# Performance work log

Hardware: AMD Instinct MI355X
Metric: run time of the kernel (lower is better)

## Reference

```python
import jax, jax.numpy as jnp
import numpy as np

SIGMA = 0.1
B = 1.0
SPATIAL_WEIGHT = 0.5
EPS = 1e-5


def setup_inputs() -> dict:
    key = jax.random.key(0)
    k1, k2 = jax.random.split(key)
    N, C, H, W = 2, 256, 64, 64
    I_features = jax.random.normal(k1, (N, C, H, W), dtype=jnp.float32)
    T_features = jax.random.normal(k2, (N, C, H, W), dtype=jnp.float32)
    return {"I_features": I_features, "T_features": T_features}


def _calc_cx(raw):
    # raw: [N, P_T, H, W]; min + exp-softmax over the target-patch axis (axis=1)
    mn = jnp.min(raw, axis=1, keepdims=True)
    rel = raw / (mn + EPS)
    w = jnp.exp((B - rel) / SIGMA)
    return w / jnp.sum(w, axis=1, keepdims=True)


def reference(I_features, T_features):
    N, C, H, W = I_features.shape
    P = H * W

    # ---- spatial branch: L2 distances on a normalized meshgrid (C=2) ----
    rows = jnp.arange(H, dtype=jnp.float32) / (H + 1)
    cols = jnp.arange(W, dtype=jnp.float32) / (W + 1)
    grid = jnp.stack(jnp.meshgrid(rows, cols, indexing="ij"))  # [2, H, W]
    g = grid.reshape(2, P)                                      # [2, P]
    sq = jnp.sum(g * g, axis=0)                                 # [P]
    d = sq[:, None] + sq[None, :] - 2.0 * (g.T @ g)             # [P_I, P_T]
    d = jnp.clip(d, 0.0)
    raw_sp = d.T.reshape(1, P, H, W)  # [1, P_T, H, W]; identical per sample
    cx_sp = _calc_cx(raw_sp)

    # ---- feature branch: cosine similarity via centered, L2-normed feats ----
    meanT = jnp.mean(T_features, axis=(0, 2, 3), keepdims=True)
    Ic = I_features - meanT
    Tc = T_features - meanT
    In = Ic / jnp.linalg.norm(Ic, axis=1, keepdims=True)
    Tn = Tc / jnp.linalg.norm(Tc, axis=1, keepdims=True)
    Iv = In.reshape(N, C, P)
    Tv = Tn.reshape(N, C, P)
    dot = jnp.einsum("ncq,ncp->nqp", Tv, Iv)  # [N, P_T, P_I]
    raw_feat = ((1.0 - dot) / 2.0).reshape(N, P, H, W)
    cx_feat = _calc_cx(raw_feat)

    # ---- combine, max over I positions, mean over T patches, -log, mean ----
    cx = (1.0 - SPATIAL_WEIGHT) * cx_feat + SPATIAL_WEIGHT * cx_sp  # [N,P,H,W]
    m = jnp.max(cx, axis=(2, 3))  # [N, P]
    m = jnp.mean(m, axis=1)       # [N]
    return jnp.mean(-jnp.log(m))
```

## Files before the change

### kernel.cpp

```cpp
#include <hip/hip_runtime.h>
#include <math.h>

#define PP 4096
#define CC 256
#define NN 2
#define QS 256
#define NSTEP (PP / QS)

typedef __attribute__((ext_vector_type(4))) float f32x4;

__device__ __forceinline__ void gld_lds16(const char* g, char* l) {
    __builtin_amdgcn_global_load_lds(
        (const __attribute__((address_space(1))) unsigned int*)g,
        (__attribute__((address_space(3))) unsigned int*)l, 16, 0, 0);
}


__global__ __launch_bounds__(256) void mean_kernel(const float* __restrict__ T,
                                                   float* __restrict__ meanT,
                                                   float* __restrict__ loss_acc) {
    int c = blockIdx.x, tid = threadIdx.x;
    float s = 0.f;
    for (int n = 0; n < NN; n++) {
        const float4* Tc = (const float4*)&T[(size_t)(n * CC + c) * PP];
        for (int g = 0; g < 4; g++) {
            float4 v = Tc[tid + g * 256];
            s += (v.x + v.y) + (v.z + v.w);
        }
    }
    __shared__ float red[256];
    red[tid] = s; __syncthreads();
    for (int st = 128; st > 0; st >>= 1) {
        if (tid < st) red[tid] += red[tid + st];
        __syncthreads();
    }
    if (tid == 0) meanT[c] = red[0] * (1.0f / (NN * PP));
    if (blockIdx.x == 0 && tid < NN) loss_acc[tid] = 0.f;
}

__global__ __launch_bounds__(256) void normalize_kernel(const float* __restrict__ I,
                                                        const float* __restrict__ T,
                                                        const float* __restrict__ meanT,
                                                        char* __restrict__ InT,
                                                        char* __restrict__ TnT) {
    int pc = blockIdx.x * 32;
    int n = blockIdx.y;
    int which = blockIdx.z;
    const float* X = which ? T : I;
    char* Y = which ? TnT : InT;

    __shared__ float tile[CC][36];
    __shared__ float red[32][32];
    __shared__ float invn[32];

    int tid = threadIdx.x;
    int pl4 = tid & 7, c0 = tid >> 3;
    float sq0 = 0.f, sq1 = 0.f, sq2 = 0.f, sq3 = 0.f;
    for (int c = c0; c < CC; c += 32) {
        float m = meanT[c];
        float4 v = *(const float4*)&X[(size_t)(n * CC + c) * PP + pc + pl4 * 4];
        v.x -= m; v.y -= m; v.z -= m; v.w -= m;
        *(float4*)&tile[c][pl4 * 4] = v;
        sq0 += v.x * v.x; sq1 += v.y * v.y; sq2 += v.z * v.z; sq3 += v.w * v.w;
    }
    red[c0][pl4 * 4 + 0] = sq0;
    red[c0][pl4 * 4 + 1] = sq1;
    red[c0][pl4 * 4 + 2] = sq2;
    red[c0][pl4 * 4 + 3] = sq3;
    __syncthreads();
    if (tid < 32) {
        float s = 0.f;
        for (int k = 0; k < 32; k++) s += red[k][tid];
        invn[tid] = 1.0f / sqrtf(s);
    }
    __syncthreads();
    for (int pass = 0; pass < 8; pass++) {
        int r = pass * 4 + (tid >> 6);
        int c4 = (tid & 63) * 4;
        float in = invn[r];
        float v0 = tile[c4 + 0][r] * in;
        float v1 = tile[c4 + 1][r] * in;
        float v2 = tile[c4 + 2][r] * in;
        float v3 = tile[c4 + 3][r] * in;
        int w = __builtin_amdgcn_cvt_pk_fp8_f32(v0, v1, 0, false);
        w = __builtin_amdgcn_cvt_pk_fp8_f32(v2, v3, w, true);
        *(unsigned*)&Y[(size_t)(n * PP + pc + r) * CC + c4] = (unsigned)w;
    }
}

__global__ __launch_bounds__(512) void cx_strip(const char* __restrict__ TnT,
                                                const char* __restrict__ InT,
                                                float* __restrict__ loss_acc) {
    const int strip = blockIdx.x;
    const int n = blockIdx.y;
    const int p0 = strip * 32;
    const char* __restrict__ Ab = TnT + (size_t)n * PP * CC;
    const char* __restrict__ Bb = InT + (size_t)n * PP * CC + (size_t)p0 * CC;

    __shared__ __align__(16) char As[2][QS * 256];
    __shared__ __align__(16) char Bs[32 * 256];
    __shared__ float redw[8][32];
    __shared__ float inv2s[32];
    __shared__ float dwl[32];

    const int tid = threadIdx.x;
    const int l = tid & 63, wv = tid >> 6;
    const int lm = l & 15, quad = l >> 4;

    const int srl = tid >> 4;
    const int sch = ((tid & 15) ^ (srl & 15)) * 16;
    const char* Asrc = Ab + srl * 256 + sch;
    char* Alds = (char*)As + tid * 16;

    gld_lds16(Bb + srl * 256 + sch, (char*)Bs + tid * 16);

    long bf[2][8];
    float cm[2] = {3.4e38f, 3.4e38f};
    float inv2[2] = {0.f, 0.f};
    float ss[2] = {0.f, 0.f};
    const int qd = p0 >> 8;
    const int wd = (p0 >> 5) & 7;

#pragma unroll 1
    for (int pass = 0; pass < 2; pass++) {
#pragma unroll
        for (int g = 0; g < 8; g++)
            gld_lds16(Asrc + g * 8192, Alds + g * 8192);
        __syncthreads();

        if (pass == 0) {
#pragma unroll
            for (int ct = 0; ct < 2; ct++)
#pragma unroll
                for (int ks = 0; ks < 8; ks++) {
                    int g8 = ks * 4 + quad;
                    int row = ct * 16 + lm;
                    bf[ct][ks] = *(const long*)&Bs[row * 256 +
                                  (((g8 >> 1) ^ (row & 15)) * 16) + (g8 & 1) * 8];
                }
        }

#pragma unroll 1
        for (int qs = 0; qs < NSTEP; qs++) {
            if (qs < NSTEP - 1) {
                const char* s = Asrc + (size_t)(qs + 1) * 65536;
                char* d = Alds + ((qs + 1) & 1) * 65536;
#pragma unroll
                for (int g = 0; g < 8; g++)
                    gld_lds16(s + g * 8192, d + g * 8192);
            }

            const char* Ac = (const char*)As + (qs & 1) * 65536;
            f32x4 acc[2][2] = {};
#pragma unroll
            for (int ks = 0; ks < 8; ks++) {
                const int off = (((ks * 2 + (quad >> 1)) ^ lm) * 16) + (quad & 1) * 8;
                long a[2];
#pragma unroll
                for (int i = 0; i < 2; i++)
                    a[i] = *(const long*)&Ac[(wv * 32 + i * 16 + lm) * 256 + off];
#pragma unroll
                for (int i = 0; i < 2; i++)
#pragma unroll
                    for (int ct = 0; ct < 2; ct++)
                        acc[i][ct] = __builtin_amdgcn_mfma_f32_16x16x32_fp8_fp8(
                            a[i], bf[ct][ks], acc[i][ct], 0, 0, 0);
            }
            if (pass == 0) {
#pragma unroll
                for (int ct = 0; ct < 2; ct++)
#pragma unroll
                    for (int i = 0; i < 2; i++)
#pragma unroll
                        for (int e = 0; e < 4; e++)
                            cm[ct] = fminf(cm[ct], (1.0f - acc[i][ct][e]) * 0.5f);
            } else {
                const bool dstep = (qs == qd) && (wv == wd);
#pragma unroll
                for (int ct = 0; ct < 2; ct++) {
                    float s2 = 0.f;
#pragma unroll
                    for (int i = 0; i < 2; i++)
#pragma unroll
                        for (int e = 0; e < 4; e++) {
                            float raw = (1.0f - acc[i][ct][e]) * 0.5f;
                            float w = exp2f(fmaf(raw, -inv2[ct], 14.4269504f));
                            s2 += w;
                            if (dstep && (i * 16 + quad * 4 + e == ct * 16 + lm))
                                dwl[ct * 16 + lm] = w;
                        }
                    ss[ct] += s2;
                }
            }
            __syncthreads();
        }

        if (pass == 0) {
#pragma unroll
            for (int ct = 0; ct < 2; ct++) {
                cm[ct] = fminf(cm[ct], __shfl_xor(cm[ct], 16));
                cm[ct] = fminf(cm[ct], __shfl_xor(cm[ct], 32));
                if (quad == 0) redw[wv][ct * 16 + lm] = cm[ct];
            }
            __syncthreads();
            if (tid < 32) {
                float m = redw[0][tid];
#pragma unroll
                for (int w2 = 1; w2 < 8; w2++) m = fminf(m, redw[w2][tid]);
                inv2s[tid] = 14.4269504f / (m + 1e-5f);
            }
            __syncthreads();
            inv2[0] = inv2s[lm];
            inv2[1] = inv2s[16 + lm];
        }
    }

#pragma unroll
    for (int ct = 0; ct < 2; ct++) {
        ss[ct] += __shfl_xor(ss[ct], 16);
        ss[ct] += __shfl_xor(ss[ct], 32);
        if (quad == 0) redw[wv][ct * 16 + lm] = ss[ct];
    }
    __syncthreads();
    if (tid < 32) {
        float s = 0.f;
#pragma unroll
        for (int w2 = 0; w2 < 8; w2++) s += redw[w2][tid];
        float part = dwl[tid] / s;
        part += __shfl_xor(part, 1);
        part += __shfl_xor(part, 2);
        part += __shfl_xor(part, 4);
        part += __shfl_xor(part, 8);
        part += __shfl_xor(part, 16);
        if (tid == 0) atomicAdd(&loss_acc[n], part);
    }
}

__global__ void finalize_kernel(const float* __restrict__ loss_acc,
                                float* __restrict__ out) {
    float m0 = 0.5f + 0.5f * (loss_acc[0] / (float)PP);
    float m1 = 0.5f + 0.5f * (loss_acc[1] / (float)PP);
    out[0] = 0.5f * (-logf(m0) - logf(m1));
}

extern "C" void kernel_launch(void* const* d_in, const int* in_sizes, int n_in,
                              void* d_out, int out_size, void* d_ws, size_t ws_size,
                              hipStream_t stream) {
    const float* I = (const float*)d_in[0];
    const float* T = (const float*)d_in[1];
    float* out = (float*)d_out;

    char* ws = (char*)d_ws;
    const size_t SZ_F8 = (size_t)NN * PP * CC;
    char* InT = ws;
    char* TnT = ws + SZ_F8;
    float* meanT = (float*)(ws + 2 * SZ_F8);
    float* loss_acc = (float*)(ws + 2 * SZ_F8 + 32768);

    mean_kernel<<<CC, 256, 0, stream>>>(T, meanT, loss_acc);
    normalize_kernel<<<dim3(PP / 32, NN, 2), 256, 0, stream>>>(I, T, meanT, InT, TnT);
    cx_strip<<<dim3(PP / 32, NN), 512, 0, stream>>>(TnT, InT, loss_acc);
    finalize_kernel<<<1, 1, 0, stream>>>(loss_acc, out);
}
```

Before: 121.9 us.

## Give each wave a private double-buffered A slice and drop per-step block barriers

```diff
diff --git a/kernel.cpp b/kernel.cpp
--- a/kernel.cpp
+++ b/kernel.cpp
@@ -4,8 +4,7 @@
 #define PP 4096
 #define CC 256
 #define NN 2
-#define QS 256
-#define NSTEP (PP / QS)
+#define NSTEP 16
 
 typedef __attribute__((ext_vector_type(4))) float f32x4;
 
@@ -97,8 +96,8 @@
     const char* __restrict__ Ab = TnT + (size_t)n * PP * CC;
     const char* __restrict__ Bb = InT + (size_t)n * PP * CC + (size_t)p0 * CC;
 
-    __shared__ __align__(16) char As[2][QS * 256];
-    __shared__ __align__(16) char Bs[32 * 256];
+    __shared__ __align__(16) char Aw[8][2][8192];
+    __shared__ __align__(16) char Bsm[8192];
     __shared__ float redw[8][32];
     __shared__ float inv2s[32];
     __shared__ float dwl[32];
@@ -106,15 +105,39 @@
     const int tid = threadIdx.x;
     const int l = tid & 63, wv = tid >> 6;
     const int lm = l & 15, quad = l >> 4;
-
-    const int srl = tid >> 4;
-    const int sch = ((tid & 15) ^ (srl & 15)) * 16;
-    const char* Asrc = Ab + srl * 256 + sch;
-    char* Alds = (char*)As + tid * 16;
-
-    gld_lds16(Bb + srl * 256 + sch, (char*)Bs + tid * 16);
+    const int lr4 = l >> 4;
+    const int sl = l & 15;
+
+#define STAGE_A(qs, b)                                                       \
+    {                                                                        \
+        const char* sbase_ = Ab + ((size_t)(qs) * 256 + wv * 32) * 256;      \
+        char* dbase_ = &Aw[wv][b][0];                                        \
+        _Pragma("unroll")                                                    \
+        for (int g_ = 0; g_ < 8; g_++) {                                     \
+            int row_ = g_ * 4 + lr4;                                         \
+            gld_lds16(sbase_ + row_ * 256 + ((sl ^ (row_ & 15)) * 16),       \
+                      dbase_ + g_ * 1024);                                   \
+        }                                                                    \
+    }
+
+    {
+        int rB = wv * 4 + lr4;
+        gld_lds16(Bb + rB * 256 + ((sl ^ (rB & 15)) * 16), &Bsm[wv * 1024]);
+    }
+    STAGE_A(0, 0);
+    __syncthreads();
 
     long bf[2][8];
+#pragma unroll
+    for (int ct = 0; ct < 2; ct++)
+#pragma unroll
+        for (int ks = 0; ks < 8; ks++) {
+            int g8 = ks * 4 + quad;
+            int row = ct * 16 + lm;
+            bf[ct][ks] = *(const long*)&Bsm[row * 256 +
+                          (((g8 >> 1) ^ (row & 15)) * 16) + (g8 & 1) * 8];
+        }
+
     float cm[2] = {3.4e38f, 3.4e38f};
     float inv2[2] = {0.f, 0.f};
     float ss[2] = {0.f, 0.f};
@@ -123,34 +146,18 @@
 
 #pragma unroll 1
     for (int pass = 0; pass < 2; pass++) {
-#pragma unroll
-        for (int g = 0; g < 8; g++)
-            gld_lds16(Asrc + g * 8192, Alds + g * 8192);
-        __syncthreads();
-
-        if (pass == 0) {
-#pragma unroll
-            for (int ct = 0; ct < 2; ct++)
-#pragma unroll
-                for (int ks = 0; ks < 8; ks++) {
-                    int g8 = ks * 4 + quad;
-                    int row = ct * 16 + lm;
-                    bf[ct][ks] = *(const long*)&Bs[row * 256 +
-                                  (((g8 >> 1) ^ (row & 15)) * 16) + (g8 & 1) * 8];
-                }
-        }
-
+        if (pass == 1) STAGE_A(0, 0);
 #pragma unroll 1
         for (int qs = 0; qs < NSTEP; qs++) {
             if (qs < NSTEP - 1) {
-                const char* s = Asrc + (size_t)(qs + 1) * 65536;
-                char* d = Alds + ((qs + 1) & 1) * 65536;
-#pragma unroll
-                for (int g = 0; g < 8; g++)
-                    gld_lds16(s + g * 8192, d + g * 8192);
-            }
-
-            const char* Ac = (const char*)As + (qs & 1) * 65536;
+                STAGE_A(qs + 1, (qs + 1) & 1);
+                asm volatile("s_waitcnt vmcnt(8)" ::: "memory");
+            } else {
+                asm volatile("s_waitcnt vmcnt(0)" ::: "memory");
+            }
+            __builtin_amdgcn_sched_barrier(0);
+
+            const char* Ac = &Aw[wv][qs & 1][0];
             f32x4 acc[2][2] = {};
 #pragma unroll
             for (int ks = 0; ks < 8; ks++) {
@@ -158,7 +165,7 @@
                 long a[2];
 #pragma unroll
                 for (int i = 0; i < 2; i++)
-                    a[i] = *(const long*)&Ac[(wv * 32 + i * 16 + lm) * 256 + off];
+                    a[i] = *(const long*)&Ac[(i * 16 + lm) * 256 + off];
 #pragma unroll
                 for (int i = 0; i < 2; i++)
 #pragma unroll
@@ -192,7 +199,6 @@
                     ss[ct] += s2;
                 }
             }
-            __syncthreads();
         }
 
         if (pass == 0) {
@@ -234,6 +240,7 @@
         part += __shfl_xor(part, 16);
         if (tid == 0) atomicAdd(&loss_acc[n], part);
     }
+#undef STAGE_A
 }
 
 __global__ void finalize_kernel(const float* __restrict__ loss_acc,
```

Result: faster. 114.6 us (-6.0%).
